# Kernel tuning notes

Measured on AMD Instinct MI355X. Metric: run time of the kernel, lower is better.

## Reference

```python
import jax, jax.numpy as jnp
import numpy as np

HIDDEN = 1024


def setup_inputs() -> dict:
    key = jax.random.key(0)
    kx, kb, kc = jax.random.split(key, 3)
    x = jax.random.normal(kx, (8, 4096, HIDDEN), dtype=jnp.float32)
    logit_a = jnp.zeros((HIDDEN,), dtype=jnp.float32)
    b = jax.random.normal(kb, (HIDDEN,), dtype=jnp.float32) * 0.1
    c = jax.random.normal(kc, (HIDDEN,), dtype=jnp.float32) * 0.1
    d = jnp.zeros((HIDDEN,), dtype=jnp.float32)
    return {"x": x, "logit_a": logit_a, "b": b, "c": c, "d": d}


def reference(x, logit_a, b, c, d):
    # x: (B, T, D); diagonal SSM: s_t = a*s_{t-1} + b*u_t ; y_t = c*s_t + d*u_t
    B, T, D = x.shape
    a = jnp.tanh(logit_a)  # (D,)

    def step(state, u_t):  # state: (B, D), u_t: (B, D)
        state = state * a + u_t * b
        y_t = state * c + u_t * d
        return state, y_t

    xs = jnp.swapaxes(x, 0, 1)  # (T, B, D)
    init = jnp.zeros((B, D), dtype=x.dtype)
    _, ys = jax.lax.scan(step, init, xs)
    return jnp.swapaxes(ys, 0, 1)  # (B, T, D)
```

## Files before the change

kernel.cpp:

```cpp
#include <hip/hip_runtime.h>
#include <math.h>


#define SSM_B 8
#define SSM_T 4096
#define SSM_D 1024
#define SSM_C 128
#define SSM_L 32

typedef float vfloat4 __attribute__((ext_vector_type(4)));

__device__ __forceinline__ float4 f4_fma(float4 a, float4 s, float4 add) {
    return make_float4(fmaf(a.x, s.x, add.x), fmaf(a.y, s.y, add.y),
                       fmaf(a.z, s.z, add.z), fmaf(a.w, s.w, add.w));
}
__device__ __forceinline__ float4 f4_mul(float4 a, float4 b) {
    return make_float4(a.x * b.x, a.y * b.y, a.z * b.z, a.w * b.w);
}
__device__ __forceinline__ void nt_store_f4(float* p, float4 w) {
    vfloat4 v = {w.x, w.y, w.z, w.w};
    __builtin_nontemporal_store(v, (vfloat4*)p);
}
__device__ __forceinline__ float4 nt_load_f4(const float* p) {
    vfloat4 v = __builtin_nontemporal_load((const vfloat4*)p);
    return make_float4(v.x, v.y, v.z, v.w);
}

__global__ __launch_bounds__(256) void ssm_pass1(
        const float* __restrict__ x, const float* __restrict__ logit_a,
        const float* __restrict__ bco, float* __restrict__ chunk_end) {
    const int k  = blockIdx.x;
    const int bb = blockIdx.y;
    const int d4 = threadIdx.x * 4;

    float4 la = *(const float4*)(logit_a + d4);
    float4 bv = *(const float4*)(bco + d4);
    float4 a  = make_float4(tanhf(la.x), tanhf(la.y), tanhf(la.z), tanhf(la.w));

    float4 s = make_float4(0.f, 0.f, 0.f, 0.f);
    const float* xp = x + ((size_t)bb * SSM_T + (size_t)k * SSM_L) * SSM_D + d4;
#pragma unroll 8
    for (int t = 0; t < SSM_L; ++t) {
        float4 u = *(const float4*)(xp + (size_t)t * SSM_D);
        s = f4_fma(a, s, f4_mul(bv, u));
    }
    *(float4*)(chunk_end + ((size_t)k * SSM_B + bb) * SSM_D + d4) = s;
}

__global__ __launch_bounds__(256) void ssm_prefix(
        const float* __restrict__ logit_a,
        const float* __restrict__ chunk_end,
        float* __restrict__ chunk_start) {
    const int tid = blockIdx.x * 256 + threadIdx.x;
    const int bb  = tid >> 10;
    const int d   = tid & (SSM_D - 1);

    float a  = tanhf(logit_a[d]);
    float aL = a;
#pragma unroll
    for (int i = 0; i < 5; ++i) aL *= aL;

    float s = 0.f;
    const size_t stride = (size_t)SSM_B * SSM_D;
    size_t idx = (size_t)bb * SSM_D + d;
#pragma unroll 4
    for (int j = 0; j < SSM_C; ++j) {
        chunk_start[idx] = s;
        s = fmaf(aL, s, chunk_end[idx]);
        idx += stride;
    }
}

__global__ __launch_bounds__(256) void ssm_pass2(
        const float* __restrict__ x, const float* __restrict__ logit_a,
        const float* __restrict__ bco, const float* __restrict__ cco,
        const float* __restrict__ dco, const float* __restrict__ chunk_start,
        float* __restrict__ y) {
    const int k  = blockIdx.x;
    const int bb = blockIdx.y;
    const int d4 = threadIdx.x * 4;

    float4 la = *(const float4*)(logit_a + d4);
    float4 bv = *(const float4*)(bco + d4);
    float4 cv = *(const float4*)(cco + d4);
    float4 dv = *(const float4*)(dco + d4);
    float4 a  = make_float4(tanhf(la.x), tanhf(la.y), tanhf(la.z), tanhf(la.w));

    float4 s = *(const float4*)(chunk_start + ((size_t)k * SSM_B + bb) * SSM_D + d4);

    const size_t base = ((size_t)bb * SSM_T + (size_t)k * SSM_L) * SSM_D + d4;
    const float* xp = x + base;
    float*       yp = y + base;
#pragma unroll 8
    for (int t = 0; t < SSM_L; ++t) {
        float4 u = nt_load_f4(xp + (size_t)t * SSM_D);
        s = f4_fma(a, s, f4_mul(bv, u));
        float4 w = f4_fma(cv, s, f4_mul(dv, u));
        nt_store_f4(yp + (size_t)t * SSM_D, w);
    }
}

extern "C" void kernel_launch(void* const* d_in, const int* in_sizes, int n_in,
                              void* d_out, int out_size, void* d_ws, size_t ws_size,
                              hipStream_t stream) {
    const float* x   = (const float*)d_in[0];
    const float* la  = (const float*)d_in[1];
    const float* bco = (const float*)d_in[2];
    const float* cco = (const float*)d_in[3];
    const float* dco = (const float*)d_in[4];
    float* y = (float*)d_out;
    float* chunk_end   = (float*)d_ws;
    float* chunk_start = (float*)d_ws + (size_t)SSM_C * SSM_B * SSM_D;

    dim3 grid(SSM_C, SSM_B);
    dim3 block(256);
    ssm_pass1<<<grid, block, 0, stream>>>(x, la, bco, chunk_end);
    ssm_prefix<<<dim3((SSM_B * SSM_D) / 256), block, 0, stream>>>(la, chunk_end, chunk_start);
    ssm_pass2<<<grid, block, 0, stream>>>(x, la, bco, cco, dco, chunk_start, y);
}
```

Before: 273.7 us.

## Fuse three SSM passes into one cooperative kernel with grid syncs

Replaces the three launches (chunk scan, prefix over chunks, final scan) with a single cooperative kernel of 512 persistent blocks that each handle two chunk tasks and separate the phases with grid-wide syncs. Pass 2 visits the tasks in reverse order so the most recently read chunk of x may still be in cache. The aim is to remove launch gaps and reuse x from cache between the passes, at the cost of grid-barrier overhead and a prefix phase that runs on only 32 blocks while the rest wait.

```diff
diff --git a/kernel.cpp b/kernel.cpp
--- a/kernel.cpp
+++ b/kernel.cpp
@@ -1,5 +1,8 @@
 #include <hip/hip_runtime.h>
+#include <hip/hip_cooperative_groups.h>
 #include <math.h>
+
+namespace cg = cooperative_groups;
 
 
 #define SSM_B 8
@@ -7,6 +10,8 @@
 #define SSM_D 1024
 #define SSM_C 128
 #define SSM_L 32
+#define NTASK (SSM_C * SSM_B)
+#define NBLK 512
 
 typedef float vfloat4 __attribute__((ext_vector_type(4)));
 
@@ -26,77 +31,73 @@
     return make_float4(v.x, v.y, v.z, v.w);
 }
 
-__global__ __launch_bounds__(256) void ssm_pass1(
+__global__ __launch_bounds__(256, 2) void ssm_fused(
         const float* __restrict__ x, const float* __restrict__ logit_a,
-        const float* __restrict__ bco, float* __restrict__ chunk_end) {
-    const int k  = blockIdx.x;
-    const int bb = blockIdx.y;
+        const float* __restrict__ bco, const float* __restrict__ cco,
+        const float* __restrict__ dco, float* __restrict__ chunk_end,
+        float* __restrict__ chunk_start, float* __restrict__ y) {
+    const int g  = blockIdx.x;
     const int d4 = threadIdx.x * 4;
 
-    float4 la = *(const float4*)(logit_a + d4);
-    float4 bv = *(const float4*)(bco + d4);
-    float4 a  = make_float4(tanhf(la.x), tanhf(la.y), tanhf(la.z), tanhf(la.w));
+    const float4 la = *(const float4*)(logit_a + d4);
+    const float4 bv = *(const float4*)(bco + d4);
+    const float4 cv = *(const float4*)(cco + d4);
+    const float4 dv = *(const float4*)(dco + d4);
+    const float4 a  = make_float4(tanhf(la.x), tanhf(la.y), tanhf(la.z), tanhf(la.w));
 
-    float4 s = make_float4(0.f, 0.f, 0.f, 0.f);
-    const float* xp = x + ((size_t)bb * SSM_T + (size_t)k * SSM_L) * SSM_D + d4;
+#pragma unroll
+    for (int i = 0; i < 2; ++i) {
+        const int tau = g + i * NBLK;
+        const int k = tau >> 3, bb = tau & 7;
+        const float* xp =
+            x + ((size_t)bb * SSM_T + (size_t)k * SSM_L) * SSM_D + d4;
+        float4 s = make_float4(0.f, 0.f, 0.f, 0.f);
 #pragma unroll 8
-    for (int t = 0; t < SSM_L; ++t) {
-        float4 u = *(const float4*)(xp + (size_t)t * SSM_D);
-        s = f4_fma(a, s, f4_mul(bv, u));
+        for (int t = 0; t < SSM_L; ++t) {
+            float4 u = *(const float4*)(xp + (size_t)t * SSM_D);
+            s = f4_fma(a, s, f4_mul(bv, u));
+        }
+        *(float4*)(chunk_end + (size_t)tau * SSM_D + d4) = s;
     }
-    *(float4*)(chunk_end + ((size_t)k * SSM_B + bb) * SSM_D + d4) = s;
-}
 
-__global__ __launch_bounds__(256) void ssm_prefix(
-        const float* __restrict__ logit_a,
-        const float* __restrict__ chunk_end,
-        float* __restrict__ chunk_start) {
-    const int tid = blockIdx.x * 256 + threadIdx.x;
-    const int bb  = tid >> 10;
-    const int d   = tid & (SSM_D - 1);
+    cg::this_grid().sync();
 
-    float a  = tanhf(logit_a[d]);
-    float aL = a;
+    if (g < (SSM_B * SSM_D) / 256) {
+        const int tid = g * 256 + threadIdx.x;
+        const int d   = tid & (SSM_D - 1);
+        float av = tanhf(logit_a[d]);
+        float aL = av;
 #pragma unroll
-    for (int i = 0; i < 5; ++i) aL *= aL;
+        for (int i = 0; i < 5; ++i) aL *= aL;
+        float s = 0.f;
+        const size_t stride = (size_t)SSM_B * SSM_D;
+        size_t idx = (size_t)tid;
+#pragma unroll 4
+        for (int j = 0; j < SSM_C; ++j) {
+            chunk_start[idx] = s;
+            s = fmaf(aL, s, chunk_end[idx]);
+            idx += stride;
+        }
+    }
 
-    float s = 0.f;
-    const size_t stride = (size_t)SSM_B * SSM_D;
-    size_t idx = (size_t)bb * SSM_D + d;
-#pragma unroll 4
-    for (int j = 0; j < SSM_C; ++j) {
-        chunk_start[idx] = s;
-        s = fmaf(aL, s, chunk_end[idx]);
-        idx += stride;
-    }
-}
+    cg::this_grid().sync();
 
-__global__ __launch_bounds__(256) void ssm_pass2(
-        const float* __restrict__ x, const float* __restrict__ logit_a,
-        const float* __restrict__ bco, const float* __restrict__ cco,
-        const float* __restrict__ dco, const float* __restrict__ chunk_start,
-        float* __restrict__ y) {
-    const int k  = blockIdx.x;
-    const int bb = blockIdx.y;
-    const int d4 = threadIdx.x * 4;
-
-    float4 la = *(const float4*)(logit_a + d4);
-    float4 bv = *(const float4*)(bco + d4);
-    float4 cv = *(const float4*)(cco + d4);
-    float4 dv = *(const float4*)(dco + d4);
-    float4 a  = make_float4(tanhf(la.x), tanhf(la.y), tanhf(la.z), tanhf(la.w));
-
-    float4 s = *(const float4*)(chunk_start + ((size_t)k * SSM_B + bb) * SSM_D + d4);
-
-    const size_t base = ((size_t)bb * SSM_T + (size_t)k * SSM_L) * SSM_D + d4;
-    const float* xp = x + base;
-    float*       yp = y + base;
+#pragma unroll
+    for (int i = 1; i >= 0; --i) {
+        const int tau = g + i * NBLK;
+        const int k = tau >> 3, bb = tau & 7;
+        float4 s = *(const float4*)(chunk_start + (size_t)tau * SSM_D + d4);
+        const size_t base =
+            ((size_t)bb * SSM_T + (size_t)k * SSM_L) * SSM_D + d4;
+        const float* xp = x + base;
+        float*       yp = y + base;
 #pragma unroll 8
-    for (int t = 0; t < SSM_L; ++t) {
-        float4 u = nt_load_f4(xp + (size_t)t * SSM_D);
-        s = f4_fma(a, s, f4_mul(bv, u));
-        float4 w = f4_fma(cv, s, f4_mul(dv, u));
-        nt_store_f4(yp + (size_t)t * SSM_D, w);
+        for (int t = 0; t < SSM_L; ++t) {
+            float4 u = nt_load_f4(xp + (size_t)t * SSM_D);
+            s = f4_fma(a, s, f4_mul(bv, u));
+            float4 w = f4_fma(cv, s, f4_mul(dv, u));
+            nt_store_f4(yp + (size_t)t * SSM_D, w);
+        }
     }
 }
 
@@ -110,11 +111,11 @@
     const float* dco = (const float*)d_in[4];
     float* y = (float*)d_out;
     float* chunk_end   = (float*)d_ws;
-    float* chunk_start = (float*)d_ws + (size_t)SSM_C * SSM_B * SSM_D;
+    float* chunk_start = (float*)d_ws + (size_t)NTASK * SSM_D;
 
-    dim3 grid(SSM_C, SSM_B);
-    dim3 block(256);
-    ssm_pass1<<<grid, block, 0, stream>>>(x, la, bco, chunk_end);
-    ssm_prefix<<<dim3((SSM_B * SSM_D) / 256), block, 0, stream>>>(la, chunk_end, chunk_start);
-    ssm_pass2<<<grid, block, 0, stream>>>(x, la, bco, cco, dco, chunk_start, y);
+    void* args[] = {(void*)&x,   (void*)&la,        (void*)&bco,
+                    (void*)&cco, (void*)&dco,       (void*)&chunk_end,
+                    (void*)&chunk_start, (void*)&y};
+    hipLaunchCooperativeKernel((void*)ssm_fused, dim3(NBLK), dim3(256), args,
+                               0, stream);
 }
```

Measured after the change: 391.5 us. 1.43x slower.
